# Kernel optimization log

Hardware: AMD Instinct MI355X
Metric: run time of the kernel (lower is better)

The kernel has to match this reference:

```python
import jax, jax.numpy as jnp
import numpy as np

EPS = 1e-07


def _pairwise_iou_xyxy(pred, tgt):
    # pred: [P,4], tgt: [T,4] in (x1,y1,x2,y2) form -> [P,T] IoU
    lt = jnp.maximum(pred[:, None, :2], tgt[None, :, :2])   # [P,T,2]
    rb = jnp.minimum(pred[:, None, 2:], tgt[None, :, 2:])   # [P,T,2]
    wh = jnp.clip(rb - lt, 0.0)                             # [P,T,2]
    inter = wh[..., 0] * wh[..., 1]                         # [P,T]
    pa = (pred[:, 2] - pred[:, 0]) * (pred[:, 3] - pred[:, 1])  # [P]
    ta = (tgt[:, 2] - tgt[:, 0]) * (tgt[:, 3] - tgt[:, 1])      # [T]
    union = pa[:, None] + ta[None, :] - inter
    return inter / (union + EPS)


def setup_inputs() -> dict:
    key = jax.random.key(0)
    k1, k2 = jax.random.split(key)
    pred_boxes = jax.random.uniform(k1, (8192, 4), dtype=jnp.float32)
    target_boxes = jax.random.uniform(k2, (4096, 4), dtype=jnp.float32)
    return {"pred_boxes": pred_boxes, "target_boxes": target_boxes}


def reference(pred_boxes, target_boxes):
    num_preds = pred_boxes.shape[0]
    num_targets = target_boxes.shape[0]
    if num_preds != num_targets:
        pairwise_ious = _pairwise_iou_xyxy(pred_boxes, target_boxes)  # [P,T]
        indices = jnp.argmax(pairwise_ious, axis=1)                    # [P]
        target_boxes = target_boxes[indices]                           # [P,4]

    # DIoU part interprets boxes as (cx, cy, w, h) -- faithful to the original
    pred_centers, pred_sizes = pred_boxes[:, :2], pred_boxes[:, 2:]
    tgt_centers, tgt_sizes = target_boxes[:, :2], target_boxes[:, 2:]

    pred_lt = pred_centers - pred_sizes / 2
    pred_rb = pred_centers + pred_sizes / 2
    tgt_lt = tgt_centers - tgt_sizes / 2
    tgt_rb = tgt_centers + tgt_sizes / 2

    inter_wh = jnp.clip(jnp.minimum(pred_rb, tgt_rb) - jnp.maximum(pred_lt, tgt_lt), 0.0)
    inter_area = inter_wh[:, 0] * inter_wh[:, 1]
    pred_area = pred_sizes[:, 0] * pred_sizes[:, 1]
    tgt_area = tgt_sizes[:, 0] * tgt_sizes[:, 1]
    iou = inter_area / (pred_area + tgt_area - inter_area + EPS)

    center_distance = jnp.sum((pred_centers - tgt_centers) ** 2, axis=1)
    enc_wh = jnp.maximum(pred_rb, tgt_rb) - jnp.minimum(pred_lt, tgt_lt)
    enc_diag = jnp.sum(enc_wh ** 2, axis=1)

    diou = iou - center_distance / (enc_diag + EPS)
    return 1.0 - jnp.mean(diou)
```

## Files before the change

### kernel.cpp

```cpp
#include <hip/hip_runtime.h>

#define EPS 1e-7f

constexpr int NPRED  = 8192;
constexpr int NTGT   = 4096;
constexpr int BLOCK  = 256;
constexpr int PW     = 4;
constexpr int PPB    = 16;
constexpr int TSPLIT = 4;
constexpr int TCHUNK = NTGT / TSPLIT;
constexpr int GRID_P = NPRED / PPB;
constexpr int GRID   = GRID_P * TSPLIT;

__device__ __forceinline__ unsigned sortable_key(float f) {
  unsigned b = __float_as_uint(f);
  return (b & 0x80000000u) ? ~b : (b | 0x80000000u);
}

__global__ __launch_bounds__(BLOCK)
void diou_argmax(const float4* __restrict__ pred,
                 const float4* __restrict__ tgt,
                 unsigned long long* __restrict__ pk) {
  __shared__ float4 sT[TCHUNK];
  const int lane  = threadIdx.x & 63;
  const int wave  = threadIdx.x >> 6;
  const int pblk  = blockIdx.x % GRID_P;
  const int tq    = blockIdx.x / GRID_P;
  const int tbase = tq * TCHUNK;
  const int pbase = pblk * PPB + wave * PW;

  for (int t = threadIdx.x; t < TCHUNK; t += BLOCK) sT[t] = tgt[tbase + t];

  float4 p[PW];
  float  paeps[PW];
  float  bestV[PW];
  int    bestI[PW];
#pragma unroll
  for (int i = 0; i < PW; ++i) {
    p[i]     = pred[pbase + i];
    paeps[i] = (p[i].z - p[i].x) * (p[i].w - p[i].y) + EPS;
    bestV[i] = -INFINITY;
    bestI[i] = 0;
  }
  __syncthreads();

  for (int t0 = 0; t0 < TCHUNK; t0 += 64) {
    const int t = t0 + lane;
    float4 tb = sT[t];
    float  ta = (tb.z - tb.x) * (tb.w - tb.y);
    int    idx = tbase + t;
#pragma unroll
    for (int i = 0; i < PW; ++i) {
      float w = fminf(p[i].z, tb.z) - fmaxf(p[i].x, tb.x);
      float h = fminf(p[i].w, tb.w) - fmaxf(p[i].y, tb.y);
      w = fmaxf(w, 0.f);
      h = fmaxf(h, 0.f);
      float inter = w * h;
      float denom = (paeps[i] + ta) - inter;
      float iou   = inter * __builtin_amdgcn_rcpf(denom);
      iou += 0.0f;
      if (iou > bestV[i]) { bestV[i] = iou; bestI[i] = idx; }
    }
  }

#pragma unroll
  for (int i = 0; i < PW; ++i) {
    float v  = bestV[i];
    int   ix = bestI[i];
    for (int off = 32; off > 0; off >>= 1) {
      float ov = __shfl_down(v, off, 64);
      int   oi = __shfl_down(ix, off, 64);
      if (ov > v || (ov == v && oi < ix)) { v = ov; ix = oi; }
    }
    if (lane == 0) {
      unsigned long long packed =
          ((unsigned long long)sortable_key(v) << 32) |
          (unsigned)(NTGT - 1 - ix);
      atomicMax(&pk[pbase + i], packed);
    }
  }
}

__global__ __launch_bounds__(BLOCK)
void diou_gather(const float4* __restrict__ pred,
                 const float4* __restrict__ tgt,
                 const unsigned long long* __restrict__ pk,
                 float* __restrict__ acc) {
  const int tid  = blockIdx.x * BLOCK + threadIdx.x;
  const int lane = threadIdx.x & 63;

  float4 p  = pred[tid];
  int    ix = NTGT - 1 - (unsigned)(pk[tid] & 0xFFFFFFFFu);
  float4 t  = tgt[ix];

  float phw = 0.5f * p.z, phh = 0.5f * p.w;
  float thw = 0.5f * t.z, thh = 0.5f * t.w;
  float pltx = p.x - phw, plty = p.y - phh;
  float prbx = p.x + phw, prby = p.y + phh;
  float tltx = t.x - thw, tlty = t.y - thh;
  float trbx = t.x + thw, trby = t.y + thh;

  float iw = fmaxf(fminf(prbx, trbx) - fmaxf(pltx, tltx), 0.f);
  float ih = fmaxf(fminf(prby, trby) - fmaxf(plty, tlty), 0.f);
  float inter = iw * ih;
  float parea = p.z * p.w;
  float tarea = t.z * t.w;
  float iou   = inter / (parea + tarea - inter + EPS);

  float dx = p.x - t.x, dy = p.y - t.y;
  float cd = dx * dx + dy * dy;

  float ew = fmaxf(prbx, trbx) - fminf(pltx, tltx);
  float eh = fmaxf(prby, trby) - fminf(plty, tlty);
  float diag = ew * ew + eh * eh;

  float v = iou - cd / (diag + EPS);

  for (int off = 32; off > 0; off >>= 1) v += __shfl_down(v, off, 64);
  if (lane == 0) atomicAdd(acc, v);
}

__global__ void diou_finalize(const float* __restrict__ acc,
                              float* __restrict__ out) {
  out[0] = 1.f - acc[0] * (1.f / (float)NPRED);
}

extern "C" void kernel_launch(void* const* d_in, const int* in_sizes, int n_in,
                              void* d_out, int out_size, void* d_ws, size_t ws_size,
                              hipStream_t stream) {
  const float4* pred = (const float4*)d_in[0];
  const float4* tgt  = (const float4*)d_in[1];

  unsigned long long* pk = (unsigned long long*)d_ws;
  float* acc = (float*)((char*)d_ws + NPRED * sizeof(unsigned long long));

  hipMemsetAsync(d_ws, 0, NPRED * sizeof(unsigned long long) + 64, stream);

  diou_argmax<<<GRID, BLOCK, 0, stream>>>(pred, tgt, pk);
  diou_gather<<<NPRED / BLOCK, BLOCK, 0, stream>>>(pred, tgt, pk, acc);
  diou_finalize<<<1, 1, 0, stream>>>(acc, (float*)d_out);
}
```

Baseline: 81.45 us.

## Fuse gather and finalize into one block, double target split in argmax

The separate gather and finalize kernels become a single 1024-thread block that computes the DIoU for all predictions, reduces through shared memory and writes the output directly. This drops one launch and the global float atomic accumulator. In the argmax kernel the target dimension is split eight ways instead of four, which doubles the grid and halves the shared tile per block. It also adds an occupancy hint and a partial unroll, and stores a local index that is offset by the chunk base at pack time. The single-block gather serialises 8192 gathers on one CU, and the wider split doubles the number of 64-bit atomics.

```diff
diff --git a/kernel.cpp b/kernel.cpp
--- a/kernel.cpp
+++ b/kernel.cpp
@@ -7,7 +7,7 @@
 constexpr int BLOCK  = 256;
 constexpr int PW     = 4;
 constexpr int PPB    = 16;
-constexpr int TSPLIT = 4;
+constexpr int TSPLIT = 8;
 constexpr int TCHUNK = NTGT / TSPLIT;
 constexpr int GRID_P = NPRED / PPB;
 constexpr int GRID   = GRID_P * TSPLIT;
@@ -17,7 +17,7 @@
   return (b & 0x80000000u) ? ~b : (b | 0x80000000u);
 }
 
-__global__ __launch_bounds__(BLOCK)
+__global__ __launch_bounds__(BLOCK, 8)
 void diou_argmax(const float4* __restrict__ pred,
                  const float4* __restrict__ tgt,
                  unsigned long long* __restrict__ pk) {
@@ -44,11 +44,11 @@
   }
   __syncthreads();
 
+#pragma unroll 4
   for (int t0 = 0; t0 < TCHUNK; t0 += 64) {
     const int t = t0 + lane;
     float4 tb = sT[t];
     float  ta = (tb.z - tb.x) * (tb.w - tb.y);
-    int    idx = tbase + t;
 #pragma unroll
     for (int i = 0; i < PW; ++i) {
       float w = fminf(p[i].z, tb.z) - fmaxf(p[i].x, tb.x);
@@ -59,7 +59,7 @@
       float denom = (paeps[i] + ta) - inter;
       float iou   = inter * __builtin_amdgcn_rcpf(denom);
       iou += 0.0f;
-      if (iou > bestV[i]) { bestV[i] = iou; bestI[i] = idx; }
+      if (iou > bestV[i]) { bestV[i] = iou; bestI[i] = t; }
     }
   }
 
@@ -75,54 +75,60 @@
     if (lane == 0) {
       unsigned long long packed =
           ((unsigned long long)sortable_key(v) << 32) |
-          (unsigned)(NTGT - 1 - ix);
+          (unsigned)(NTGT - 1 - (tbase + ix));
       atomicMax(&pk[pbase + i], packed);
     }
   }
 }
 
-__global__ __launch_bounds__(BLOCK)
-void diou_gather(const float4* __restrict__ pred,
-                 const float4* __restrict__ tgt,
-                 const unsigned long long* __restrict__ pk,
-                 float* __restrict__ acc) {
-  const int tid  = blockIdx.x * BLOCK + threadIdx.x;
-  const int lane = threadIdx.x & 63;
+__global__ __launch_bounds__(1024)
+void diou_gather_finalize(const float4* __restrict__ pred,
+                          const float4* __restrict__ tgt,
+                          const unsigned long long* __restrict__ pk,
+                          float* __restrict__ out) {
+  __shared__ float sP[16];
+  const int tid  = threadIdx.x;
+  const int lane = tid & 63;
 
-  float4 p  = pred[tid];
-  int    ix = NTGT - 1 - (unsigned)(pk[tid] & 0xFFFFFFFFu);
-  float4 t  = tgt[ix];
+  float v = 0.f;
+  for (int j = tid; j < NPRED; j += 1024) {
+    float4 p  = pred[j];
+    int    ix = NTGT - 1 - (int)(unsigned)(pk[j] & 0xFFFFFFFFu);
+    float4 t  = tgt[ix];
 
-  float phw = 0.5f * p.z, phh = 0.5f * p.w;
-  float thw = 0.5f * t.z, thh = 0.5f * t.w;
-  float pltx = p.x - phw, plty = p.y - phh;
-  float prbx = p.x + phw, prby = p.y + phh;
-  float tltx = t.x - thw, tlty = t.y - thh;
-  float trbx = t.x + thw, trby = t.y + thh;
+    float phw = 0.5f * p.z, phh = 0.5f * p.w;
+    float thw = 0.5f * t.z, thh = 0.5f * t.w;
+    float pltx = p.x - phw, plty = p.y - phh;
+    float prbx = p.x + phw, prby = p.y + phh;
+    float tltx = t.x - thw, tlty = t.y - thh;
+    float trbx = t.x + thw, trby = t.y + thh;
 
-  float iw = fmaxf(fminf(prbx, trbx) - fmaxf(pltx, tltx), 0.f);
-  float ih = fmaxf(fminf(prby, trby) - fmaxf(plty, tlty), 0.f);
-  float inter = iw * ih;
-  float parea = p.z * p.w;
-  float tarea = t.z * t.w;
-  float iou   = inter / (parea + tarea - inter + EPS);
+    float iw = fmaxf(fminf(prbx, trbx) - fmaxf(pltx, tltx), 0.f);
+    float ih = fmaxf(fminf(prby, trby) - fmaxf(plty, tlty), 0.f);
+    float inter = iw * ih;
+    float parea = p.z * p.w;
+    float tarea = t.z * t.w;
+    float iou   = inter / (parea + tarea - inter + EPS);
 
-  float dx = p.x - t.x, dy = p.y - t.y;
-  float cd = dx * dx + dy * dy;
+    float dx = p.x - t.x, dy = p.y - t.y;
+    float cd = dx * dx + dy * dy;
 
-  float ew = fmaxf(prbx, trbx) - fminf(pltx, tltx);
-  float eh = fmaxf(prby, trby) - fminf(plty, tlty);
-  float diag = ew * ew + eh * eh;
+    float ew = fmaxf(prbx, trbx) - fminf(pltx, tltx);
+    float eh = fmaxf(prby, trby) - fminf(plty, tlty);
+    float diag = ew * ew + eh * eh;
 
-  float v = iou - cd / (diag + EPS);
+    v += iou - cd / (diag + EPS);
+  }
 
   for (int off = 32; off > 0; off >>= 1) v += __shfl_down(v, off, 64);
-  if (lane == 0) atomicAdd(acc, v);
-}
-
-__global__ void diou_finalize(const float* __restrict__ acc,
-                              float* __restrict__ out) {
-  out[0] = 1.f - acc[0] * (1.f / (float)NPRED);
+  if (lane == 0) sP[tid >> 6] = v;
+  __syncthreads();
+  if (tid == 0) {
+    float s = 0.f;
+#pragma unroll
+    for (int i = 0; i < 16; ++i) s += sP[i];
+    out[0] = 1.f - s * (1.f / (float)NPRED);
+  }
 }
 
 extern "C" void kernel_launch(void* const* d_in, const int* in_sizes, int n_in,
@@ -130,13 +136,9 @@
                               hipStream_t stream) {
   const float4* pred = (const float4*)d_in[0];
   const float4* tgt  = (const float4*)d_in[1];
+  unsigned long long* pk = (unsigned long long*)d_ws;
 
-  unsigned long long* pk = (unsigned long long*)d_ws;
-  float* acc = (float*)((char*)d_ws + NPRED * sizeof(unsigned long long));
-
-  hipMemsetAsync(d_ws, 0, NPRED * sizeof(unsigned long long) + 64, stream);
-
+  hipMemsetAsync(pk, 0, NPRED * sizeof(unsigned long long), stream);
   diou_argmax<<<GRID, BLOCK, 0, stream>>>(pred, tgt, pk);
-  diou_gather<<<NPRED / BLOCK, BLOCK, 0, stream>>>(pred, tgt, pk, acc);
-  diou_finalize<<<1, 1, 0, stream>>>(acc, (float*)d_out);
+  diou_gather_finalize<<<1, 1024, 0, stream>>>(pred, tgt, pk, (float*)d_out);
 }
```

Result: slower. 83.57 us (+2.6%).

## Fold finalize into gather via last-block counter and trim argmax inner loop

Applied to the files above, without the earlier changes.

Removes the separate single-thread finalize kernel: the gather kernel reduces per block through shared memory and the last block, detected with an atomic counter, writes the final loss. The argmax kernel now tracks a local index and adds the chunk base only once at the end, moves the negative-zero normalisation out of the hot loop, unrolls the target loop and sets a launch-bounds occupancy hint. This saves one kernel launch and some per-iteration ALU work. The trade-off is a threadfence and counter protocol that relies on the memset zeroing the counter on every call.

```diff
diff --git a/kernel.cpp b/kernel.cpp
--- a/kernel.cpp
+++ b/kernel.cpp
@@ -11,13 +11,14 @@
 constexpr int TCHUNK = NTGT / TSPLIT;
 constexpr int GRID_P = NPRED / PPB;
 constexpr int GRID   = GRID_P * TSPLIT;
+constexpr int GBLK   = 32;
 
 __device__ __forceinline__ unsigned sortable_key(float f) {
   unsigned b = __float_as_uint(f);
   return (b & 0x80000000u) ? ~b : (b | 0x80000000u);
 }
 
-__global__ __launch_bounds__(BLOCK)
+__global__ __launch_bounds__(BLOCK, 8)
 void diou_argmax(const float4* __restrict__ pred,
                  const float4* __restrict__ tgt,
                  unsigned long long* __restrict__ pk) {
@@ -29,6 +30,7 @@
   const int tbase = tq * TCHUNK;
   const int pbase = pblk * PPB + wave * PW;
 
+#pragma unroll
   for (int t = threadIdx.x; t < TCHUNK; t += BLOCK) sT[t] = tgt[tbase + t];
 
   float4 p[PW];
@@ -44,11 +46,11 @@
   }
   __syncthreads();
 
+#pragma unroll 4
   for (int t0 = 0; t0 < TCHUNK; t0 += 64) {
     const int t = t0 + lane;
     float4 tb = sT[t];
     float  ta = (tb.z - tb.x) * (tb.w - tb.y);
-    int    idx = tbase + t;
 #pragma unroll
     for (int i = 0; i < PW; ++i) {
       float w = fminf(p[i].z, tb.z) - fmaxf(p[i].x, tb.x);
@@ -58,8 +60,7 @@
       float inter = w * h;
       float denom = (paeps[i] + ta) - inter;
       float iou   = inter * __builtin_amdgcn_rcpf(denom);
-      iou += 0.0f;
-      if (iou > bestV[i]) { bestV[i] = iou; bestI[i] = idx; }
+      if (iou > bestV[i]) { bestV[i] = iou; bestI[i] = t; }
     }
   }
 
@@ -73,9 +74,10 @@
       if (ov > v || (ov == v && oi < ix)) { v = ov; ix = oi; }
     }
     if (lane == 0) {
+      v += 0.0f;
       unsigned long long packed =
           ((unsigned long long)sortable_key(v) << 32) |
-          (unsigned)(NTGT - 1 - ix);
+          (unsigned)(NTGT - 1 - (tbase + ix));
       atomicMax(&pk[pbase + i], packed);
     }
   }
@@ -85,12 +87,16 @@
 void diou_gather(const float4* __restrict__ pred,
                  const float4* __restrict__ tgt,
                  const unsigned long long* __restrict__ pk,
-                 float* __restrict__ acc) {
+                 float* __restrict__ acc,
+                 unsigned* __restrict__ cnt,
+                 float* __restrict__ out) {
+  __shared__ float sP[4];
   const int tid  = blockIdx.x * BLOCK + threadIdx.x;
   const int lane = threadIdx.x & 63;
+  const int wave = threadIdx.x >> 6;
 
   float4 p  = pred[tid];
-  int    ix = NTGT - 1 - (unsigned)(pk[tid] & 0xFFFFFFFFu);
+  int    ix = NTGT - 1 - (int)(unsigned)(pk[tid] & 0xFFFFFFFFu);
   float4 t  = tgt[ix];
 
   float phw = 0.5f * p.z, phh = 0.5f * p.w;
@@ -117,12 +123,16 @@
   float v = iou - cd / (diag + EPS);
 
   for (int off = 32; off > 0; off >>= 1) v += __shfl_down(v, off, 64);
-  if (lane == 0) atomicAdd(acc, v);
-}
-
-__global__ void diou_finalize(const float* __restrict__ acc,
-                              float* __restrict__ out) {
-  out[0] = 1.f - acc[0] * (1.f / (float)NPRED);
+  if (lane == 0) sP[wave] = v;
+  __syncthreads();
+  if (threadIdx.x == 0) {
+    atomicAdd(acc, sP[0] + sP[1] + sP[2] + sP[3]);
+    __threadfence();
+    if (atomicAdd(cnt, 1u) == GBLK - 1) {
+      float s = atomicAdd(acc, 0.0f);
+      out[0] = 1.f - s * (1.f / (float)NPRED);
+    }
+  }
 }
 
 extern "C" void kernel_launch(void* const* d_in, const int* in_sizes, int n_in,
@@ -132,11 +142,10 @@
   const float4* tgt  = (const float4*)d_in[1];
 
   unsigned long long* pk = (unsigned long long*)d_ws;
-  float* acc = (float*)((char*)d_ws + NPRED * sizeof(unsigned long long));
+  float*    acc = (float*)   ((char*)d_ws + NPRED * 8);
+  unsigned* cnt = (unsigned*)((char*)d_ws + NPRED * 8 + 4);
 
-  hipMemsetAsync(d_ws, 0, NPRED * sizeof(unsigned long long) + 64, stream);
-
+  hipMemsetAsync(d_ws, 0, NPRED * 8 + 8, stream);
   diou_argmax<<<GRID, BLOCK, 0, stream>>>(pred, tgt, pk);
-  diou_gather<<<NPRED / BLOCK, BLOCK, 0, stream>>>(pred, tgt, pk, acc);
-  diou_finalize<<<1, 1, 0, stream>>>(acc, (float*)d_out);
+  diou_gather<<<GBLK, BLOCK, 0, stream>>>(pred, tgt, pk, acc, cnt, (float*)d_out);
 }
```

Measured after the change: 80.37 us. Within noise of the previous version (-1.3%).
